# Performance work log

Hardware: AMD Instinct MI355X
Metric: run time of the kernel (lower is better)

The kernel has to match this reference:

```python
import jax, jax.numpy as jnp
import numpy as np
import math

N, D, H, DK, DV, FF = 2048, 1024, 16, 64, 64, 4096
EPS = 1e-5


def setup_inputs() -> dict:
    key = jax.random.key(0)
    ks = jax.random.split(key, 10)
    s = 0.02  # scaled init for numerical stability (original uses torch.randn)
    return {
        "x": jax.random.normal(ks[0], (N, D), dtype=jnp.float32),
        # per-head projections stacked: [H, D, DK/DV]
        "w_q": jax.random.normal(ks[1], (H, D, DK), dtype=jnp.float32) * s,
        "w_k": jax.random.normal(ks[2], (H, D, DK), dtype=jnp.float32) * s,
        "w_v": jax.random.normal(ks[3], (H, D, DV), dtype=jnp.float32) * s,
        "w_o": jax.random.normal(ks[4], (H * DV, D), dtype=jnp.float32) * s,
        "ln1_g": jnp.ones((D,), jnp.float32),
        "ln1_b": jnp.zeros((D,), jnp.float32),
        # FFN: Linear stored as [in, out] so y = x @ w + b
        "w1": jax.random.normal(ks[5], (D, FF), dtype=jnp.float32) * s,
        "b1": jnp.zeros((FF,), jnp.float32),
        "w2": jax.random.normal(ks[6], (FF, D), dtype=jnp.float32) * s,
        "b2": jnp.zeros((D,), jnp.float32),
        "ln2_g": jnp.ones((D,), jnp.float32),
        "ln2_b": jnp.zeros((D,), jnp.float32),
    }


def _layernorm(x, g, b):
    mu = jnp.mean(x, axis=-1, keepdims=True)
    var = jnp.mean(jnp.square(x - mu), axis=-1, keepdims=True)
    return (x - mu) * jax.lax.rsqrt(var + EPS) * g + b


def reference(x, w_q, w_k, w_v, w_o, ln1_g, ln1_b, w1, b1, w2, b2, ln2_g, ln2_b):
    n = x.shape[0]
    # multi-head causal self-attention (heads batched instead of Python loop)
    q = jnp.einsum('nd,hdk->hnk', x, w_q)  # [H,N,DK]
    k = jnp.einsum('nd,hdk->hnk', x, w_k)
    v = jnp.einsum('nd,hdv->hnv', x, w_v)
    scores = jnp.einsum('hnk,hmk->hnm', q, k) / math.sqrt(DK)  # [H,N,N]
    causal = jnp.tril(jnp.ones((n, n), dtype=bool))
    scores = jnp.where(causal, scores, -jnp.inf)
    probs = jax.nn.softmax(scores, axis=-1)
    attn = jnp.einsum('hnm,hmv->hnv', probs, v)  # [H,N,DV]
    concat = jnp.transpose(attn, (1, 0, 2)).reshape(n, H * DV)  # head-order concat
    mha = concat @ w_o  # [N,D]
    # residual + LN, FFN (note: ReLU after BOTH linears, as in the source)
    h = _layernorm(x + mha, ln1_g, ln1_b)
    ff = jax.nn.relu(jax.nn.relu(h @ w1 + b1) @ w2 + b2)
    return _layernorm(h + ff, ln2_g, ln2_b)
```

## Files before the change

kernel.cpp:

```cpp
#include <hip/hip_runtime.h>
#include <math.h>


#define NTOK   2048
#define DMODEL 1024
#define NHEAD  16
#define DHEAD  64
#define DFF    4096
#define LNEPS  1e-5f

typedef unsigned int   u32;
typedef unsigned short u16;
typedef __attribute__((ext_vector_type(8))) short short8;
typedef __attribute__((ext_vector_type(4))) float f32x4;

__device__ __forceinline__ u16 f2b(float f) {
    u32 b = __float_as_uint(f);
    b += 0x7FFFu + ((b >> 16) & 1u);
    return (u16)(b >> 16);
}

#define AS1(p) ((const __attribute__((address_space(1))) u32*)(p))
#define AS3(p) ((__attribute__((address_space(3))) u32*)(p))

template<int RELU, int BIAS, int RESID, int OUT_BF16, int SPLITK>
__global__ __launch_bounds__(256) void mfma_gemm(
    const u16* __restrict__ A, int lda,
    const u16* __restrict__ Bt, int ldbt,
    void* __restrict__ Cp, int ldc, int Kc,
    const float* __restrict__ bias,
    const float* __restrict__ resid, int ldr,
    size_t pstride)
{
    __shared__ u16 As[2][128 * 32];
    __shared__ u16 Bs[2][128 * 32];

    const int tid = threadIdx.x;
    const int l = tid & 63, w = tid >> 6;
    const int row0 = blockIdx.y * 128, col0 = blockIdx.x * 128;
    const int kbase = (SPLITK > 1) ? blockIdx.z * Kc : 0;

    f32x4 acc[4][4];
    #pragma unroll
    for (int m = 0; m < 4; ++m)
        #pragma unroll
        for (int n = 0; n < 4; ++n)
            acc[m][n] = (f32x4){0.f, 0.f, 0.f, 0.f};

    const int srow = w * 32 + (l >> 2);
    const int skk  = (l & 3) * 8;
    const u16* Ag = A  + (size_t)(row0 + srow) * lda  + kbase + skk;
    const u16* Bg = Bt + (size_t)(col0 + srow) * ldbt + kbase + skk;

    const int fr  = l & 15;
    const int fk  = (l >> 4) * 8;
    const int ar0 = (w >> 1) * 64;
    const int bc0 = (w & 1) * 64;

    auto STAGE = [&](int buf, int k0) {
        char* AsB = (char*)&As[buf][0] + w * 2048;
        char* BsB = (char*)&Bs[buf][0] + w * 2048;
        __builtin_amdgcn_global_load_lds(AS1(Ag + k0),                     AS3(AsB),        16, 0, 0);
        __builtin_amdgcn_global_load_lds(AS1(Ag + k0 + (size_t)16 * lda),  AS3(AsB + 1024), 16, 0, 0);
        __builtin_amdgcn_global_load_lds(AS1(Bg + k0),                     AS3(BsB),        16, 0, 0);
        __builtin_amdgcn_global_load_lds(AS1(Bg + k0 + (size_t)16 * ldbt), AS3(BsB + 1024), 16, 0, 0);
    };

    STAGE(0, 0);
    int cur = 0;
    for (int k0 = 0; k0 < Kc; k0 += 32) {
        __syncthreads();
        if (k0 + 32 < Kc) STAGE(cur ^ 1, k0 + 32);

        short8 af[4], bfr[4];
        #pragma unroll
        for (int m = 0; m < 4; ++m)
            af[m] = *reinterpret_cast<const short8*>(&As[cur][(ar0 + m * 16 + fr) * 32 + fk]);
        #pragma unroll
        for (int n = 0; n < 4; ++n)
            bfr[n] = *reinterpret_cast<const short8*>(&Bs[cur][(bc0 + n * 16 + fr) * 32 + fk]);
        #pragma unroll
        for (int m = 0; m < 4; ++m)
            #pragma unroll
            for (int n = 0; n < 4; ++n)
                acc[m][n] = __builtin_amdgcn_mfma_f32_16x16x32_bf16(af[m], bfr[n], acc[m][n], 0, 0, 0);
        cur ^= 1;
    }

    if (SPLITK > 1) {
        float* Pp = (float*)Cp + blockIdx.z * pstride;
        #pragma unroll
        for (int m = 0; m < 4; ++m)
            #pragma unroll
            for (int n = 0; n < 4; ++n)
                #pragma unroll
                for (int r = 0; r < 4; ++r) {
                    int row = row0 + ar0 + m * 16 + (l >> 4) * 4 + r;
                    int col = col0 + bc0 + n * 16 + (l & 15);
                    Pp[(size_t)row * ldc + col] = acc[m][n][r];
                }
        return;
    }

    #pragma unroll
    for (int m = 0; m < 4; ++m) {
        #pragma unroll
        for (int n = 0; n < 4; ++n) {
            #pragma unroll
            for (int r = 0; r < 4; ++r) {
                int row = row0 + ar0 + m * 16 + (l >> 4) * 4 + r;
                int col = col0 + bc0 + n * 16 + (l & 15);
                float val = acc[m][n][r];
                if (BIAS)  val += bias[col];
                if (RESID) val += resid[(size_t)row * ldr + col];
                if (RELU)  val = fmaxf(val, 0.0f);
                if (OUT_BF16) ((u16*)Cp)[(size_t)row * ldc + col] = f2b(val);
                else          ((float*)Cp)[(size_t)row * ldc + col] = val;
            }
        }
    }
}

__global__ __launch_bounds__(256) void cast_f32_bf16(const float* __restrict__ in,
                                                     u16* __restrict__ out, int n)
{
    int i = (blockIdx.x * 256 + threadIdx.x) * 4;
    if (i + 3 < n) {
        float4 v = *reinterpret_cast<const float4*>(in + i);
        ushort4 o;
        o.x = f2b(v.x); o.y = f2b(v.y); o.z = f2b(v.z); o.w = f2b(v.w);
        *reinterpret_cast<ushort4*>(out + i) = o;
    }
}

__device__ __forceinline__ void transpose_body(const float* __restrict__ in, int ldin,
                                               u16* __restrict__ out, int ldout)
{
    __shared__ float tile[32][33];
    int r0 = blockIdx.y * 32, c0 = blockIdx.x * 32;
    int tx = threadIdx.x & 31, ty = threadIdx.x >> 5;
    #pragma unroll
    for (int i = 0; i < 4; ++i) {
        int r = ty + i * 8;
        tile[r][tx] = in[(size_t)(r0 + r) * ldin + c0 + tx];
    }
    __syncthreads();
    #pragma unroll
    for (int i = 0; i < 4; ++i) {
        int rr = ty + i * 8;
        out[(size_t)(c0 + rr) * ldout + r0 + tx] = f2b(tile[tx][rr]);
    }
}

__global__ __launch_bounds__(256) void transpose_cast(const float* __restrict__ in, int ldin,
                                                      u16* __restrict__ out, int ldout)
{
    transpose_body(in, ldin, out, ldout);
}

__global__ __launch_bounds__(256) void cast_wqkv(
    const float* __restrict__ wq, const float* __restrict__ wk, const float* __restrict__ wv,
    u16* __restrict__ outT)
{
    int z = blockIdx.z, p = z >> 4, h = z & 15;
    const float* in = (p == 0 ? wq : p == 1 ? wk : wv) + (size_t)h * DMODEL * DHEAD;
    u16* out = outT + (size_t)(p * 1024 + h * 64) * DMODEL;
    transpose_body(in, DHEAD, out, DMODEL);
}

__global__ __launch_bounds__(512) void flash_attn_mfma(
    const u16* __restrict__ qkvb, u16* __restrict__ concatb)
{
    const int bid = blockIdx.x;
    const int lo = bid & 255;
    int it = lo >> 3;
    int h  = lo & 7;
    if (bid >= 256) { it = 31 - it; h += 8; }

    const u16* qh = qkvb + h * DHEAD;
    const u16* kh = qkvb + DMODEL + h * DHEAD;
    const u16* vh = qkvb + 2 * DMODEL + h * DHEAD;
    const int LDQ = 3 * DMODEL;

    __shared__ u16 Ks[2][64][72];
    __shared__ u16 Vt[2][64][72];

    const int tid = threadIdx.x;
    const int l = tid & 63, w = tid >> 6;
    const int grp = w >> 2, wq = w & 3;
    const int fr = l & 15, fg = l >> 4;

    short8 qf[2];
    {
        const u16* qp = qh + (size_t)(it * 64 + wq * 16 + fr) * LDQ + fg * 8;
        qf[0] = *reinterpret_cast<const short8*>(qp);
        qf[1] = *reinterpret_cast<const short8*>(qp + 32);
    }

    const int kr  = tid >> 2;
    const int kb  = kr >> 6, krl = kr & 63;
    const int kc  = (tid & 3) * 16;
    const int vp  = tid >> 3;
    const int vb  = vp >> 5, vpl = vp & 31;
    const int vc  = (tid & 7) * 8;

    short8 kf0, kf1, vf0, vf1;
    auto PREFETCH = [&](int s) {
        const u16* kg = kh + (size_t)(s * 128 + kr) * LDQ + kc;
        kf0 = *reinterpret_cast<const short8*>(kg);
        kf1 = *reinterpret_cast<const short8*>(kg + 8);
        const u16* vg = vh + (size_t)(s * 128 + 2 * vp) * LDQ + vc;
        vf0 = *reinterpret_cast<const short8*>(vg);
        vf1 = *reinterpret_cast<const short8*>(vg + LDQ);
    };

    f32x4 o[4];
    #pragma unroll
    for (int n = 0; n < 4; ++n) o[n] = (f32x4){0.f, 0.f, 0.f, 0.f};
    float m_run = -INFINITY, l_run = 0.0f;

    const int sA = fr + 16 * ((2 * fg) & 3);
    const int sB = sA + 16;
    const bool hi = (fg >= 2);

    const u16 (*KsG)[72] = Ks[grp];
    char* VtG = (char*)&Vt[grp][0][0];
    char* VtS = (char*)&Vt[vb][0][0];

    const int niter = (it >> 1) + 1;
    PREFETCH(0);

    for (int s = 0; s < niter; ++s) {
        __syncthreads();
        *reinterpret_cast<short8*>(&Ks[kb][krl][kc])     = kf0;
        *reinterpret_cast<short8*>(&Ks[kb][krl][kc + 8]) = kf1;
        #pragma unroll
        for (int i = 0; i < 8; ++i) {
            u32 word = (u32)(u16)vf0[i] | ((u32)(u16)vf1[i] << 16);
            int dv = vc + i;
            int off = 144 * dv + 16 * ((vpl >> 2) ^ ((dv >> 3) & 7)) + 4 * (vpl & 3);
            *reinterpret_cast<u32*>(VtS + off) = word;
        }
        if (s + 1 < niter) PREFETCH(s + 1);
        __syncthreads();

        const int jt = 2 * s + grp;
        if (jt > it) continue;

        f32x4 s_[4];
        #pragma unroll
        for (int n = 0; n < 4; ++n) s_[n] = (f32x4){0.f, 0.f, 0.f, 0.f};
        __builtin_amdgcn_s_setprio(1);
        #pragma unroll
        for (int n = 0; n < 4; ++n) {
            #pragma unroll
            for (int ks = 0; ks < 2; ++ks) {
                short8 kfrag = *reinterpret_cast<const short8*>(&KsG[n * 16 + fr][ks * 32 + fg * 8]);
                s_[n] = __builtin_amdgcn_mfma_f32_16x16x32_bf16(kfrag, qf[ks], s_[n], 0, 0, 0);
            }
        }
        __builtin_amdgcn_s_setprio(0);

        const bool diag = (jt == it);
        const int qrow_t = wq * 16 + fr;
        float sv[4][4];
        float pm = -INFINITY;
        #pragma unroll
        for (int n = 0; n < 4; ++n)
            #pragma unroll
            for (int r = 0; r < 4; ++r) {
                float v = s_[n][r] * 0.125f;
                if (diag && (n * 16 + fg * 4 + r) > qrow_t) v = -INFINITY;
                sv[n][r] = v;
                pm = fmaxf(pm, v);
            }
        pm = fmaxf(pm, __shfl_xor(pm, 16));
        pm = fmaxf(pm, __shfl_xor(pm, 32));
        float mnew = fmaxf(m_run, pm);
        float corr = __expf(m_run - mnew);
        float rs = 0.0f;
        float pp[4][4];
        #pragma unroll
        for (int n = 0; n < 4; ++n)
            #pragma unroll
            for (int r = 0; r < 4; ++r) {
                float pv = __expf(sv[n][r] - mnew);
                pp[n][r] = pv;
                rs += pv;
            }
        rs += __shfl_xor(rs, 16);
        rs += __shfl_xor(rs, 32);
        l_run = l_run * corr + rs;
        m_run = mnew;
        #pragma unroll
        for (int n = 0; n < 4; ++n) {
            o[n][0] *= corr; o[n][1] *= corr; o[n][2] *= corr; o[n][3] *= corr;
        }

        u32 pk[4][2];
        #pragma unroll
        for (int n = 0; n < 4; ++n) {
            pk[n][0] = (__float_as_uint(pp[n][0]) >> 16) | (__float_as_uint(pp[n][1]) & 0xFFFF0000u);
            pk[n][1] = (__float_as_uint(pp[n][2]) >> 16) | (__float_as_uint(pp[n][3]) & 0xFFFF0000u);
        }

        __builtin_amdgcn_s_setprio(1);
        #pragma unroll
        for (int ks = 0; ks < 2; ++ks) {
            u32 a0 = __shfl(pk[2 * ks][0], sA);
            u32 a1 = __shfl(pk[2 * ks][1], sA);
            u32 a2 = __shfl(pk[2 * ks][0], sB);
            u32 a3 = __shfl(pk[2 * ks][1], sB);
            u32 b0 = __shfl(pk[2 * ks + 1][0], sA);
            u32 b1 = __shfl(pk[2 * ks + 1][1], sA);
            u32 b2 = __shfl(pk[2 * ks + 1][0], sB);
            u32 b3 = __shfl(pk[2 * ks + 1][1], sB);
            union { u32 u[4]; short8 s8; } pb;
            pb.u[0] = hi ? b0 : a0;
            pb.u[1] = hi ? b1 : a1;
            pb.u[2] = hi ? b2 : a2;
            pb.u[3] = hi ? b3 : a3;
            #pragma unroll
            for (int n = 0; n < 4; ++n) {
                int dv = n * 16 + fr;
                const short8* vfrag = reinterpret_cast<const short8*>(
                    VtG + 144 * dv + 16 * ((ks * 4 + fg) ^ ((dv >> 3) & 7)));
                o[n] = __builtin_amdgcn_mfma_f32_16x16x32_bf16(*vfrag, pb.s8, o[n], 0, 0, 0);
            }
        }
        __builtin_amdgcn_s_setprio(0);
    }

    __syncthreads();
    float* mrg = reinterpret_cast<float*>(&Ks[0][0][0]);
    const int slot = (wq * 64 + l) * 18;
    if (grp == 1) {
        #pragma unroll
        for (int n = 0; n < 4; ++n)
            #pragma unroll
            for (int r = 0; r < 4; ++r)
                mrg[slot + n * 4 + r] = o[n][r];
        mrg[slot + 16] = m_run;
        mrg[slot + 17] = l_run;
    }
    __syncthreads();
    if (grp == 0) {
        float mB = mrg[slot + 16], lB = mrg[slot + 17];
        float mstar = fmaxf(m_run, mB);
        float cA = __expf(m_run - mstar);
        float cB = __expf(mB - mstar);
        float inv = 1.0f / (l_run * cA + lB * cB);
        int qrow = it * 64 + wq * 16 + fr;
        #pragma unroll
        for (int n = 0; n < 4; ++n)
            #pragma unroll
            for (int r = 0; r < 4; ++r) {
                float val = (o[n][r] * cA + mrg[slot + n * 4 + r] * cB) * inv;
                concatb[(size_t)qrow * DMODEL + h * DHEAD + n * 16 + fg * 4 + r] = f2b(val);
            }
    }
}

template<int NPART, int RELUB, int DUAL>
__global__ __launch_bounds__(256) void ln_fuse(
    const float* __restrict__ P, size_t pstride,
    const float* __restrict__ base,
    const float* __restrict__ bias2,
    const float* __restrict__ g, const float* __restrict__ b,
    float* __restrict__ out, u16* __restrict__ outb)
{
    int row = blockIdx.x, tid = threadIdx.x;
    __shared__ float red[256];
    size_t off = (size_t)row * DMODEL + tid * 4;

    float4 acc = *reinterpret_cast<const float4*>(P + off);
    #pragma unroll
    for (int p = 1; p < NPART; ++p) {
        float4 t = *reinterpret_cast<const float4*>(P + (size_t)p * pstride + off);
        acc.x += t.x; acc.y += t.y; acc.z += t.z; acc.w += t.w;
    }
    if (RELUB) {
        float4 bb = *reinterpret_cast<const float4*>(bias2 + tid * 4);
        acc.x = fmaxf(acc.x + bb.x, 0.0f); acc.y = fmaxf(acc.y + bb.y, 0.0f);
        acc.z = fmaxf(acc.z + bb.z, 0.0f); acc.w = fmaxf(acc.w + bb.w, 0.0f);
    }
    float4 bs = *reinterpret_cast<const float4*>(base + off);
    float vals[4] = {acc.x + bs.x, acc.y + bs.y, acc.z + bs.z, acc.w + bs.w};

    float s = vals[0] + vals[1] + vals[2] + vals[3];
    red[tid] = s; __syncthreads();
    for (int st = 128; st > 0; st >>= 1) { if (tid < st) red[tid] += red[tid + st]; __syncthreads(); }
    float mu = red[0] * (1.0f / DMODEL);
    __syncthreads();

    float vs = 0.0f;
    #pragma unroll
    for (int i = 0; i < 4; ++i) { float d = vals[i] - mu; vs += d * d; }
    red[tid] = vs; __syncthreads();
    for (int st = 128; st > 0; st >>= 1) { if (tid < st) red[tid] += red[tid + st]; __syncthreads(); }
    float rstd = rsqrtf(red[0] * (1.0f / DMODEL) + LNEPS);

    float4 gv = *reinterpret_cast<const float4*>(g + tid * 4);
    float4 bv = *reinterpret_cast<const float4*>(b + tid * 4);
    float gs[4] = {gv.x, gv.y, gv.z, gv.w};
    float bsc[4] = {bv.x, bv.y, bv.z, bv.w};
    #pragma unroll
    for (int i = 0; i < 4; ++i) {
        float r = (vals[i] - mu) * rstd * gs[i] + bsc[i];
        out[off + i] = r;
        if (DUAL) outb[off + i] = f2b(r);
    }
}

extern "C" void kernel_launch(void* const* d_in, const int* in_sizes, int n_in,
                              void* d_out, int out_size, void* d_ws, size_t ws_size,
                              hipStream_t stream)
{
    const float* x    = (const float*)d_in[0];
    const float* wq   = (const float*)d_in[1];
    const float* wk   = (const float*)d_in[2];
    const float* wv   = (const float*)d_in[3];
    const float* wo   = (const float*)d_in[4];
    const float* ln1g = (const float*)d_in[5];
    const float* ln1b = (const float*)d_in[6];
    const float* w1   = (const float*)d_in[7];
    const float* b1   = (const float*)d_in[8];
    const float* w2   = (const float*)d_in[9];
    const float* b2   = (const float*)d_in[10];
    const float* ln2g = (const float*)d_in[11];
    const float* ln2b = (const float*)d_in[12];
    float* out = (float*)d_out;

    char* ws = (char*)d_ws;
    const size_t MB = 1024 * 1024;
    u16*   w2T     = (u16*)  (ws + 0 * MB);
    float* h1      = (float*)(ws + 8 * MB);
    float* P01     = (float*)(ws + 16 * MB);
    u16*   ff1b    = (u16*)  (ws + 16 * MB);
    float* FP      = (float*)(ws + 32 * MB);
    u16*   wqkvT   = (u16*)  (ws + 32 * MB);
    u16*   woT     = (u16*)  (ws + 38 * MB);
    u16*   w1T     = (u16*)  (ws + 40 * MB);
    u16*   xb      = (u16*)  (ws + 48 * MB);
    u16*   concatb = (u16*)  (ws + 48 * MB);
    u16*   h1b     = (u16*)  (ws + 48 * MB);
    u16*   qkvb    = (u16*)  (ws + 52 * MB);

    const size_t PSTRIDE = (size_t)NTOK * DMODEL;

    dim3 blk(256);

    cast_f32_bf16<<<dim3(NTOK * DMODEL / 1024), blk, 0, stream>>>(x, xb, NTOK * DMODEL);
    cast_wqkv<<<dim3(2, 32, 48), blk, 0, stream>>>(wq, wk, wv, wqkvT);
    transpose_cast<<<dim3(32, 32),  blk, 0, stream>>>(wo, DMODEL, woT, DMODEL);
    transpose_cast<<<dim3(128, 32), blk, 0, stream>>>(w1, DFF, w1T, DMODEL);
    transpose_cast<<<dim3(32, 128), blk, 0, stream>>>(w2, DMODEL, w2T, DFF);

    mfma_gemm<0,0,0,1,1><<<dim3(24, 16), blk, 0, stream>>>(
        xb, DMODEL, wqkvT, DMODEL, qkvb, 3 * DMODEL, DMODEL, nullptr, nullptr, 0, 0);
    flash_attn_mfma<<<dim3(512), dim3(512), 0, stream>>>(qkvb, concatb);
    mfma_gemm<0,0,0,0,2><<<dim3(8, 16, 2), blk, 0, stream>>>(
        concatb, DMODEL, woT, DMODEL, P01, DMODEL, 512, nullptr, nullptr, 0, PSTRIDE);
    ln_fuse<2,0,1><<<dim3(NTOK), blk, 0, stream>>>(
        P01, PSTRIDE, x, nullptr, ln1g, ln1b, h1, h1b);
    mfma_gemm<1,1,0,1,1><<<dim3(32, 16), blk, 0, stream>>>(
        h1b, DMODEL, w1T, DMODEL, ff1b, DFF, DMODEL, b1, nullptr, 0, 0);
    mfma_gemm<0,0,0,0,4><<<dim3(8, 16, 4), blk, 0, stream>>>(
        ff1b, DFF, w2T, DFF, FP, DMODEL, 1024, nullptr, nullptr, 0, PSTRIDE);
    ln_fuse<4,1,0><<<dim3(NTOK), blk, 0, stream>>>(
        FP, PSTRIDE, h1, b2, ln2g, ln2b, out, nullptr);
}
```

Before: 174.8 us.

## Merge prep kernels into one launch and widen flash-attention KV stage

Folds the five input-cast and weight-transpose launches into one prep_all kernel that dispatches on block index, removing launch gaps. In flash attention, each loop iteration now loads 256 keys into four LDS buffers, and each warp group processes two tiles per sync, halving the barrier count. It also adds a lazy rescale that skips the output correction unless the row max grows by more than 8. This doubles LDS use per block and adds register pressure from wider prefetches, which may reduce occupancy.

```diff
diff --git a/kernel.cpp b/kernel.cpp
--- a/kernel.cpp
+++ b/kernel.cpp
@@ -121,23 +121,11 @@
     }
 }
 
-__global__ __launch_bounds__(256) void cast_f32_bf16(const float* __restrict__ in,
-                                                     u16* __restrict__ out, int n)
-{
-    int i = (blockIdx.x * 256 + threadIdx.x) * 4;
-    if (i + 3 < n) {
-        float4 v = *reinterpret_cast<const float4*>(in + i);
-        ushort4 o;
-        o.x = f2b(v.x); o.y = f2b(v.y); o.z = f2b(v.z); o.w = f2b(v.w);
-        *reinterpret_cast<ushort4*>(out + i) = o;
-    }
-}
-
-__device__ __forceinline__ void transpose_body(const float* __restrict__ in, int ldin,
-                                               u16* __restrict__ out, int ldout)
+__device__ __forceinline__ void transpose_tile32(
+    const float* __restrict__ in, int ldin,
+    u16* __restrict__ out, int ldout, int r0, int c0)
 {
     __shared__ float tile[32][33];
-    int r0 = blockIdx.y * 32, c0 = blockIdx.x * 32;
     int tx = threadIdx.x & 31, ty = threadIdx.x >> 5;
     #pragma unroll
     for (int i = 0; i < 4; ++i) {
@@ -152,20 +140,40 @@
     }
 }
 
-__global__ __launch_bounds__(256) void transpose_cast(const float* __restrict__ in, int ldin,
-                                                      u16* __restrict__ out, int ldout)
-{
-    transpose_body(in, ldin, out, ldout);
-}
-
-__global__ __launch_bounds__(256) void cast_wqkv(
+__global__ __launch_bounds__(256) void prep_all(
+    const float* __restrict__ x,
     const float* __restrict__ wq, const float* __restrict__ wk, const float* __restrict__ wv,
-    u16* __restrict__ outT)
-{
-    int z = blockIdx.z, p = z >> 4, h = z & 15;
-    const float* in = (p == 0 ? wq : p == 1 ? wk : wv) + (size_t)h * DMODEL * DHEAD;
-    u16* out = outT + (size_t)(p * 1024 + h * 64) * DMODEL;
-    transpose_body(in, DHEAD, out, DMODEL);
+    const float* __restrict__ wo, const float* __restrict__ w1, const float* __restrict__ w2,
+    u16* __restrict__ xb, u16* __restrict__ wqkvT, u16* __restrict__ woT,
+    u16* __restrict__ w1T, u16* __restrict__ w2T)
+{
+    int b = blockIdx.x;
+    if (b < 1024) {
+        int i = (b * 256 + threadIdx.x) * 8;
+        float4 v0 = *reinterpret_cast<const float4*>(x + i);
+        float4 v1 = *reinterpret_cast<const float4*>(x + i + 4);
+        ushort4 o0, o1;
+        o0.x = f2b(v0.x); o0.y = f2b(v0.y); o0.z = f2b(v0.z); o0.w = f2b(v0.w);
+        o1.x = f2b(v1.x); o1.y = f2b(v1.y); o1.z = f2b(v1.z); o1.w = f2b(v1.w);
+        *reinterpret_cast<ushort4*>(xb + i)     = o0;
+        *reinterpret_cast<ushort4*>(xb + i + 4) = o1;
+    } else if (b < 4096) {
+        int u = b - 1024;
+        int z = u >> 6, t = u & 63;
+        int p = z >> 4, hh = z & 15;
+        const float* in = (p == 0 ? wq : p == 1 ? wk : wv) + (size_t)hh * DMODEL * DHEAD;
+        u16* out = wqkvT + (size_t)(p * 1024 + hh * 64) * DMODEL;
+        transpose_tile32(in, DHEAD, out, DMODEL, (t >> 1) * 32, (t & 1) * 32);
+    } else if (b < 5120) {
+        int u = b - 4096;
+        transpose_tile32(wo, DMODEL, woT, DMODEL, (u >> 5) * 32, (u & 31) * 32);
+    } else if (b < 9216) {
+        int u = b - 5120;
+        transpose_tile32(w1, DFF, w1T, DMODEL, (u >> 7) * 32, (u & 127) * 32);
+    } else {
+        int u = b - 9216;
+        transpose_tile32(w2, DMODEL, w2T, DFF, (u >> 5) * 32, (u & 31) * 32);
+    }
 }
 
 __global__ __launch_bounds__(512) void flash_attn_mfma(
@@ -182,8 +190,8 @@
     const u16* vh = qkvb + 2 * DMODEL + h * DHEAD;
     const int LDQ = 3 * DMODEL;
 
-    __shared__ u16 Ks[2][64][72];
-    __shared__ u16 Vt[2][64][72];
+    __shared__ u16 Ks[4][64][72];
+    __shared__ u16 Vt[4][64][72];
 
     const int tid = threadIdx.x;
     const int l = tid & 63, w = tid >> 6;
@@ -197,21 +205,25 @@
         qf[1] = *reinterpret_cast<const short8*>(qp + 32);
     }
 
-    const int kr  = tid >> 2;
+    const int kr  = tid >> 1;
     const int kb  = kr >> 6, krl = kr & 63;
-    const int kc  = (tid & 3) * 16;
-    const int vp  = tid >> 3;
+    const int kc  = (tid & 1) * 32;
+    const int vp  = tid >> 2;
     const int vb  = vp >> 5, vpl = vp & 31;
-    const int vc  = (tid & 7) * 8;
-
-    short8 kf0, kf1, vf0, vf1;
+    const int vc  = (tid & 3) * 16;
+
+    short8 kf[4], vf0[2], vf1[2];
     auto PREFETCH = [&](int s) {
-        const u16* kg = kh + (size_t)(s * 128 + kr) * LDQ + kc;
-        kf0 = *reinterpret_cast<const short8*>(kg);
-        kf1 = *reinterpret_cast<const short8*>(kg + 8);
-        const u16* vg = vh + (size_t)(s * 128 + 2 * vp) * LDQ + vc;
-        vf0 = *reinterpret_cast<const short8*>(vg);
-        vf1 = *reinterpret_cast<const short8*>(vg + LDQ);
+        const u16* kg = kh + (size_t)(s * 256 + kr) * LDQ + kc;
+        kf[0] = *reinterpret_cast<const short8*>(kg);
+        kf[1] = *reinterpret_cast<const short8*>(kg + 8);
+        kf[2] = *reinterpret_cast<const short8*>(kg + 16);
+        kf[3] = *reinterpret_cast<const short8*>(kg + 24);
+        const u16* vg = vh + (size_t)(s * 256 + 2 * vp) * LDQ + vc;
+        vf0[0] = *reinterpret_cast<const short8*>(vg);
+        vf0[1] = *reinterpret_cast<const short8*>(vg + 8);
+        vf1[0] = *reinterpret_cast<const short8*>(vg + LDQ);
+        vf1[1] = *reinterpret_cast<const short8*>(vg + LDQ + 8);
     };
 
     f32x4 o[4];
@@ -223,112 +235,124 @@
     const int sB = sA + 16;
     const bool hi = (fg >= 2);
 
-    const u16 (*KsG)[72] = Ks[grp];
-    char* VtG = (char*)&Vt[grp][0][0];
-    char* VtS = (char*)&Vt[vb][0][0];
-
-    const int niter = (it >> 1) + 1;
+    char* VtSb = (char*)&Vt[vb][0][0];
+
+    const int niter = (it >> 2) + 1;
     PREFETCH(0);
 
     for (int s = 0; s < niter; ++s) {
         __syncthreads();
-        *reinterpret_cast<short8*>(&Ks[kb][krl][kc])     = kf0;
-        *reinterpret_cast<short8*>(&Ks[kb][krl][kc + 8]) = kf1;
-        #pragma unroll
-        for (int i = 0; i < 8; ++i) {
-            u32 word = (u32)(u16)vf0[i] | ((u32)(u16)vf1[i] << 16);
-            int dv = vc + i;
-            int off = 144 * dv + 16 * ((vpl >> 2) ^ ((dv >> 3) & 7)) + 4 * (vpl & 3);
-            *reinterpret_cast<u32*>(VtS + off) = word;
+        *reinterpret_cast<short8*>(&Ks[kb][krl][kc +  0]) = kf[0];
+        *reinterpret_cast<short8*>(&Ks[kb][krl][kc +  8]) = kf[1];
+        *reinterpret_cast<short8*>(&Ks[kb][krl][kc + 16]) = kf[2];
+        *reinterpret_cast<short8*>(&Ks[kb][krl][kc + 24]) = kf[3];
+        #pragma unroll
+        for (int c2 = 0; c2 < 2; ++c2) {
+            #pragma unroll
+            for (int i = 0; i < 8; ++i) {
+                u32 word = (u32)(u16)vf0[c2][i] | ((u32)(u16)vf1[c2][i] << 16);
+                int dv = vc + c2 * 8 + i;
+                int off = 144 * dv + 16 * ((vpl >> 2) ^ ((dv >> 3) & 7)) + 4 * (vpl & 3);
+                *reinterpret_cast<u32*>(VtSb + off) = word;
+            }
         }
         if (s + 1 < niter) PREFETCH(s + 1);
         __syncthreads();
 
-        const int jt = 2 * s + grp;
-        if (jt > it) continue;
-
-        f32x4 s_[4];
-        #pragma unroll
-        for (int n = 0; n < 4; ++n) s_[n] = (f32x4){0.f, 0.f, 0.f, 0.f};
-        __builtin_amdgcn_s_setprio(1);
-        #pragma unroll
-        for (int n = 0; n < 4; ++n) {
+        #pragma unroll
+        for (int t = 0; t < 2; ++t) {
+            const int jt = 4 * s + 2 * grp + t;
+            if (jt > it) continue;
+            const int buf = 2 * grp + t;
+            const u16 (*KsG)[72] = Ks[buf];
+            char* VtG = (char*)&Vt[buf][0][0];
+
+            f32x4 s_[4];
+            #pragma unroll
+            for (int n = 0; n < 4; ++n) s_[n] = (f32x4){0.f, 0.f, 0.f, 0.f};
+            __builtin_amdgcn_s_setprio(1);
+            #pragma unroll
+            for (int n = 0; n < 4; ++n) {
+                #pragma unroll
+                for (int ks = 0; ks < 2; ++ks) {
+                    short8 kfrag = *reinterpret_cast<const short8*>(&KsG[n * 16 + fr][ks * 32 + fg * 8]);
+                    s_[n] = __builtin_amdgcn_mfma_f32_16x16x32_bf16(kfrag, qf[ks], s_[n], 0, 0, 0);
+                }
+            }
+            __builtin_amdgcn_s_setprio(0);
+
+            const bool diag = (jt == it);
+            const int qrow_t = wq * 16 + fr;
+            float sv[4][4];
+            float pm = -INFINITY;
+            #pragma unroll
+            for (int n = 0; n < 4; ++n)
+                #pragma unroll
+                for (int r = 0; r < 4; ++r) {
+                    float v = s_[n][r] * 0.125f;
+                    if (diag && (n * 16 + fg * 4 + r) > qrow_t) v = -INFINITY;
+                    sv[n][r] = v;
+                    pm = fmaxf(pm, v);
+                }
+            pm = fmaxf(pm, __shfl_xor(pm, 16));
+            pm = fmaxf(pm, __shfl_xor(pm, 32));
+            if (!__all(pm <= m_run + 8.0f)) {
+                float mnew = fmaxf(m_run, pm);
+                float corr = __expf(m_run - mnew);
+                l_run *= corr;
+                #pragma unroll
+                for (int n = 0; n < 4; ++n) {
+                    o[n][0] *= corr; o[n][1] *= corr; o[n][2] *= corr; o[n][3] *= corr;
+                }
+                m_run = mnew;
+            }
+            float rs = 0.0f;
+            float pp[4][4];
+            #pragma unroll
+            for (int n = 0; n < 4; ++n)
+                #pragma unroll
+                for (int r = 0; r < 4; ++r) {
+                    float pv = __expf(sv[n][r] - m_run);
+                    pp[n][r] = pv;
+                    rs += pv;
+                }
+            rs += __shfl_xor(rs, 16);
+            rs += __shfl_xor(rs, 32);
+            l_run += rs;
+
+            u32 pk[4][2];
+            #pragma unroll
+            for (int n = 0; n < 4; ++n) {
+                pk[n][0] = (__float_as_uint(pp[n][0]) >> 16) | (__float_as_uint(pp[n][1]) & 0xFFFF0000u);
+                pk[n][1] = (__float_as_uint(pp[n][2]) >> 16) | (__float_as_uint(pp[n][3]) & 0xFFFF0000u);
+            }
+
+            __builtin_amdgcn_s_setprio(1);
             #pragma unroll
             for (int ks = 0; ks < 2; ++ks) {
-                short8 kfrag = *reinterpret_cast<const short8*>(&KsG[n * 16 + fr][ks * 32 + fg * 8]);
-                s_[n] = __builtin_amdgcn_mfma_f32_16x16x32_bf16(kfrag, qf[ks], s_[n], 0, 0, 0);
-            }
+                u32 a0 = __shfl(pk[2 * ks][0], sA);
+                u32 a1 = __shfl(pk[2 * ks][1], sA);
+                u32 a2 = __shfl(pk[2 * ks][0], sB);
+                u32 a3 = __shfl(pk[2 * ks][1], sB);
+                u32 b0 = __shfl(pk[2 * ks + 1][0], sA);
+                u32 b1 = __shfl(pk[2 * ks + 1][1], sA);
+                u32 b2 = __shfl(pk[2 * ks + 1][0], sB);
+                u32 b3 = __shfl(pk[2 * ks + 1][1], sB);
+                union { u32 u[4]; short8 s8; } pb;
+                pb.u[0] = hi ? b0 : a0;
+                pb.u[1] = hi ? b1 : a1;
+                pb.u[2] = hi ? b2 : a2;
+                pb.u[3] = hi ? b3 : a3;
+                #pragma unroll
+                for (int n = 0; n < 4; ++n) {
+                    int dv = n * 16 + fr;
+                    const short8* vfrag = reinterpret_cast<const short8*>(
+                        VtG + 144 * dv + 16 * ((ks * 4 + fg) ^ ((dv >> 3) & 7)));
+                    o[n] = __builtin_amdgcn_mfma_f32_16x16x32_bf16(*vfrag, pb.s8, o[n], 0, 0, 0);
+                }
+            }
+            __builtin_amdgcn_s_setprio(0);
         }
-        __builtin_amdgcn_s_setprio(0);
-
-        const bool diag = (jt == it);
-        const int qrow_t = wq * 16 + fr;
-        float sv[4][4];
-        float pm = -INFINITY;
-        #pragma unroll
-        for (int n = 0; n < 4; ++n)
-            #pragma unroll
-            for (int r = 0; r < 4; ++r) {
-                float v = s_[n][r] * 0.125f;
-                if (diag && (n * 16 + fg * 4 + r) > qrow_t) v = -INFINITY;
-                sv[n][r] = v;
-                pm = fmaxf(pm, v);
-            }
-        pm = fmaxf(pm, __shfl_xor(pm, 16));
-        pm = fmaxf(pm, __shfl_xor(pm, 32));
-        float mnew = fmaxf(m_run, pm);
-        float corr = __expf(m_run - mnew);
-        float rs = 0.0f;
-        float pp[4][4];
-        #pragma unroll
-        for (int n = 0; n < 4; ++n)
-            #pragma unroll
-            for (int r = 0; r < 4; ++r) {
-                float pv = __expf(sv[n][r] - mnew);
-                pp[n][r] = pv;
-                rs += pv;
-            }
-        rs += __shfl_xor(rs, 16);
-        rs += __shfl_xor(rs, 32);
-        l_run = l_run * corr + rs;
-        m_run = mnew;
-        #pragma unroll
-        for (int n = 0; n < 4; ++n) {
-            o[n][0] *= corr; o[n][1] *= corr; o[n][2] *= corr; o[n][3] *= corr;
-        }
-
-        u32 pk[4][2];
-        #pragma unroll
-        for (int n = 0; n < 4; ++n) {
-            pk[n][0] = (__float_as_uint(pp[n][0]) >> 16) | (__float_as_uint(pp[n][1]) & 0xFFFF0000u);
-            pk[n][1] = (__float_as_uint(pp[n][2]) >> 16) | (__float_as_uint(pp[n][3]) & 0xFFFF0000u);
-        }
-
-        __builtin_amdgcn_s_setprio(1);
-        #pragma unroll
-        for (int ks = 0; ks < 2; ++ks) {
-            u32 a0 = __shfl(pk[2 * ks][0], sA);
-            u32 a1 = __shfl(pk[2 * ks][1], sA);
-            u32 a2 = __shfl(pk[2 * ks][0], sB);
-            u32 a3 = __shfl(pk[2 * ks][1], sB);
-            u32 b0 = __shfl(pk[2 * ks + 1][0], sA);
-            u32 b1 = __shfl(pk[2 * ks + 1][1], sA);
-            u32 b2 = __shfl(pk[2 * ks + 1][0], sB);
-            u32 b3 = __shfl(pk[2 * ks + 1][1], sB);
-            union { u32 u[4]; short8 s8; } pb;
-            pb.u[0] = hi ? b0 : a0;
-            pb.u[1] = hi ? b1 : a1;
-            pb.u[2] = hi ? b2 : a2;
-            pb.u[3] = hi ? b3 : a3;
-            #pragma unroll
-            for (int n = 0; n < 4; ++n) {
-                int dv = n * 16 + fr;
-                const short8* vfrag = reinterpret_cast<const short8*>(
-                    VtG + 144 * dv + 16 * ((ks * 4 + fg) ^ ((dv >> 3) & 7)));
-                o[n] = __builtin_amdgcn_mfma_f32_16x16x32_bf16(*vfrag, pb.s8, o[n], 0, 0, 0);
-            }
-        }
-        __builtin_amdgcn_s_setprio(0);
     }
 
     __syncthreads();
@@ -450,11 +474,8 @@
 
     dim3 blk(256);
 
-    cast_f32_bf16<<<dim3(NTOK * DMODEL / 1024), blk, 0, stream>>>(x, xb, NTOK * DMODEL);
-    cast_wqkv<<<dim3(2, 32, 48), blk, 0, stream>>>(wq, wk, wv, wqkvT);
-    transpose_cast<<<dim3(32, 32),  blk, 0, stream>>>(wo, DMODEL, woT, DMODEL);
-    transpose_cast<<<dim3(128, 32), blk, 0, stream>>>(w1, DFF, w1T, DMODEL);
-    transpose_cast<<<dim3(32, 128), blk, 0, stream>>>(w2, DMODEL, w2T, DFF);
+    prep_all<<<dim3(13312), blk, 0, stream>>>(x, wq, wk, wv, wo, w1, w2,
+                                              xb, wqkvT, woT, w1T, w2T);
 
     mfma_gemm<0,0,0,1,1><<<dim3(24, 16), blk, 0, stream>>>(
         xb, DMODEL, wqkvT, DMODEL, qkvb, 3 * DMODEL, DMODEL, nullptr, nullptr, 0, 0);
```

Result: faster. 166.6 us (-4.7%).
